# Performance work log

Hardware: AMD Instinct MI355X
Metric: run time of the kernel (lower is better)

The kernel has to match this reference:

```python
import jax, jax.numpy as jnp
import numpy as np

B, N, C, DIN, DOUT = 16, 65536, 256, 16, 16  # ratio = N // C = 256 nodes per cluster


def setup_inputs() -> dict:
    key = jax.random.key(0)
    k1, k2, k3, k4, k5 = jax.random.split(key, 5)
    stdv = 1.0 / np.sqrt(DOUT)
    x = jax.random.normal(k1, (B, N, DIN), dtype=jnp.float32)
    # parameters, pre-reshaped: torch w_diag (in*out, C) with out-major io axis -> (out, in, C)
    w_diag = jax.random.uniform(k2, (DOUT, DIN, C), jnp.float32, -stdv, stdv)
    w_off = jax.random.uniform(k3, (DOUT, DIN, C, C), jnp.float32, -stdv, stdv)
    b1 = jax.random.uniform(k4, (DOUT,), jnp.float32, -stdv, stdv)
    # flatten_ids(cluster_ids): a permutation putting each cluster's nodes contiguous
    permute_ids = jax.random.permutation(k5, N)
    return {"x": x, "w_diag": w_diag, "w_off": w_off, "b1": b1, "permute_ids": permute_ids}


def reference(x, w_diag, w_off, b1, permute_ids):
    # Faithful to: W = rearrange(kron(diag_embed(w_diag), I_r)) + (1/N) rearrange(kron(w_off, 1_{rxr}))
    # out = inv_permute( reshape( W @ flatten(permute(x)) ) ) + b1,
    # computed via the block-constant structure instead of materializing the (Dout*N, Din*N) W.
    Bq, Nn, Din = x.shape
    Dout, _, Cc = w_diag.shape
    ratio = Nn // Cc
    inv_permute = jnp.argsort(permute_ids)
    xp = x[:, permute_ids, :]                       # (B, N, Din), cluster-contiguous
    xc = xp.reshape(Bq, Cc, ratio, Din)             # (B, C, r, Din)
    # diagonal blocks: per-cluster Din->Dout mixing, identity over within-cluster index
    out_diag = jnp.einsum('oic,bcri->bcro', w_diag, xc)   # (B, C, r, Dout)
    # off blocks: constant within each (cluster j, cluster k) block -> use cluster sums
    s = xc.sum(axis=2)                              # (B, C, Din)
    out_off = jnp.einsum('oick,bki->bco', w_off, s) / Nn  # (B, C, Dout)
    out = out_diag + out_off[:, :, None, :]         # broadcast over within-cluster index
    out = out.reshape(Bq, Nn, Dout)[:, inv_permute, :] + b1[None, None, :]
    return out
```

## Files before the change

kernel.cpp:

```cpp
#include <hip/hip_runtime.h>

#define B_    16
#define N_    65536
#define C_    256
#define DIN_  16
#define DOUT_ 16
#define RATIO_ 256


__global__ __launch_bounds__(256) void k_cluster_sum(
    const float* __restrict__ x, const float* __restrict__ w_diag,
    const int* __restrict__ P, float* __restrict__ s, float* __restrict__ wd_t)
{
    int bid = blockIdx.x;
    int t = threadIdx.x;
    if (bid >= B_ * C_) {
        int c = bid - B_ * C_;
        int i = t >> 4, o = t & 15;
        wd_t[c * 256 + t] = w_diag[(o * DIN_ + i) * C_ + c];
        return;
    }
    int b = bid >> 8;
    int k = bid & (C_ - 1);
    int q  = t & 3;
    int rg = t >> 2;
    float4 acc = make_float4(0.f, 0.f, 0.f, 0.f);
    const int jbase = k * RATIO_;
    #pragma unroll
    for (int m = 0; m < 4; ++m) {
        int n = P[jbase + rg + 64 * m];
        const float4* row =
            reinterpret_cast<const float4*>(x + ((size_t)(b * N_ + n)) * DIN_);
        float4 v = row[q];
        acc.x += v.x; acc.y += v.y; acc.z += v.z; acc.w += v.w;
    }
    #pragma unroll
    for (int mask = 4; mask <= 32; mask <<= 1) {
        acc.x += __shfl_xor(acc.x, mask, 64);
        acc.y += __shfl_xor(acc.y, mask, 64);
        acc.z += __shfl_xor(acc.z, mask, 64);
        acc.w += __shfl_xor(acc.w, mask, 64);
    }
    __shared__ float4 part[4][4];
    int lane = t & 63, wave = t >> 6;
    if (lane < 4) part[wave][lane] = acc;
    __syncthreads();
    if (t < 16) {
        int qq = t >> 2, comp = t & 3;
        float v = 0.f;
        #pragma unroll
        for (int w = 0; w < 4; ++w) {
            const float* p = reinterpret_cast<const float*>(&part[w][qq]);
            v += p[comp];
        }
        int i = qq * 4 + comp;
        s[i * (B_ * C_) + b * C_ + k] = v;
    }
}

__global__ __launch_bounds__(256) void k_off(
    const float* __restrict__ w_off, const float* __restrict__ s,
    const float* __restrict__ b1, float* __restrict__ off)
{
    int c  = blockIdx.x >> 2;
    int og = blockIdx.x & 3;
    int t  = threadIdx.x;
    float acc[64];
    #pragma unroll
    for (int z = 0; z < 64; ++z) acc[z] = 0.f;

    for (int i = 0; i < DIN_; ++i) {
        float wv[4];
        #pragma unroll
        for (int o4 = 0; o4 < 4; ++o4) {
            int o = og * 4 + o4;
            wv[o4] = w_off[((size_t)((o * DIN_ + i) * C_ + c)) * C_ + t];
        }
        #pragma unroll
        for (int b = 0; b < B_; ++b) {
            float sv = s[i * (B_ * C_) + b * C_ + t];
            #pragma unroll
            for (int o4 = 0; o4 < 4; ++o4) acc[b * 4 + o4] += wv[o4] * sv;
        }
    }

    __shared__ float red[8][256];
    const float invN = 1.0f / (float)N_;
    #pragma unroll
    for (int rd = 0; rd < 8; ++rd) {
        __syncthreads();
        #pragma unroll
        for (int oo = 0; oo < 8; ++oo) red[oo][t] = acc[rd * 8 + oo];
        __syncthreads();
        int grp = t >> 5;
        int seg = t & 31;
        float p = 0.f;
        #pragma unroll
        for (int j = 0; j < 8; ++j) p += red[grp][seg * 8 + j];
        #pragma unroll
        for (int d = 16; d > 0; d >>= 1) p += __shfl_down(p, d, 32);
        if (seg == 0) {
            int outid = rd * 8 + grp;
            int b  = outid >> 2, o4 = outid & 3;
            int o  = og * 4 + o4;
            off[((b << 8) + c) * DOUT_ + o] = p * invN + b1[o];
        }
    }
}

__global__ __launch_bounds__(256) void k_apply(
    const float* __restrict__ x, const int* __restrict__ P,
    const float* __restrict__ wd_t, const float* __restrict__ off,
    float* __restrict__ out)
{
    int bid = blockIdx.x;
    int b = bid >> 8, k = bid & (C_ - 1);
    int t = threadIdx.x;
    __shared__ float4 wds[64];
    __shared__ float4 offs[4];
    reinterpret_cast<float*>(wds)[t] = wd_t[k * 256 + t];
    if (t < 16)
        reinterpret_cast<float*>(offs)[t] = off[((b << 8) + k) * DOUT_ + t];
    __syncthreads();

    int n = P[(k << 8) + t];
    const float4* row =
        reinterpret_cast<const float4*>(x + ((size_t)(b * N_ + n)) * DIN_);
    float4 x0 = row[0], x1 = row[1], x2 = row[2], x3 = row[3];
    float xv[16];
    xv[0]=x0.x; xv[1]=x0.y; xv[2]=x0.z; xv[3]=x0.w;
    xv[4]=x1.x; xv[5]=x1.y; xv[6]=x1.z; xv[7]=x1.w;
    xv[8]=x2.x; xv[9]=x2.y; xv[10]=x2.z; xv[11]=x2.w;
    xv[12]=x3.x; xv[13]=x3.y; xv[14]=x3.z; xv[15]=x3.w;

    float4 a0 = offs[0], a1 = offs[1], a2 = offs[2], a3 = offs[3];
    #pragma unroll
    for (int i = 0; i < 16; ++i) {
        float xi = xv[i];
        float4 w0 = wds[i * 4 + 0];
        float4 w1 = wds[i * 4 + 1];
        float4 w2 = wds[i * 4 + 2];
        float4 w3 = wds[i * 4 + 3];
        a0.x += xi * w0.x; a0.y += xi * w0.y; a0.z += xi * w0.z; a0.w += xi * w0.w;
        a1.x += xi * w1.x; a1.y += xi * w1.y; a1.z += xi * w1.z; a1.w += xi * w1.w;
        a2.x += xi * w2.x; a2.y += xi * w2.y; a2.z += xi * w2.z; a2.w += xi * w2.w;
        a3.x += xi * w3.x; a3.y += xi * w3.y; a3.z += xi * w3.z; a3.w += xi * w3.w;
    }
    float4* orow =
        reinterpret_cast<float4*>(out + ((size_t)(b * N_ + n)) * DOUT_);
    orow[0] = a0; orow[1] = a1; orow[2] = a2; orow[3] = a3;
}

extern "C" void kernel_launch(void* const* d_in, const int* in_sizes, int n_in,
                              void* d_out, int out_size, void* d_ws, size_t ws_size,
                              hipStream_t stream) {
    const float* x      = (const float*)d_in[0];
    const float* w_diag = (const float*)d_in[1];
    const float* w_off  = (const float*)d_in[2];
    const float* b1     = (const float*)d_in[3];
    const int*   P      = (const int*)d_in[4];
    float* out  = (float*)d_out;
    float* s    = (float*)d_ws;
    float* off  = s + 65536;
    float* wd_t = off + 65536;

    k_cluster_sum<<<B_ * C_ + C_, 256, 0, stream>>>(x, w_diag, P, s, wd_t);
    k_off<<<C_ * 4, 256, 0, stream>>>(w_off, s, b1, off);
    k_apply<<<B_ * C_, 256, 0, stream>>>(x, P, wd_t, off, out);
}
```

Before: 230.0 us.

## Fuse cluster sum into diagonal apply pass and add off-block term afterward

Merges the cluster-sum kernel with the diagonal Din->Dout apply so x is gathered only once, computing cluster sums from the same loaded rows via wave shuffles. The off-block contribution is then added in a separate streaming pass that uses a precomputed node-to-cluster map. This removes one gathered read of x but adds a full read-modify-write pass over the output plus a prep kernel building the inverse cluster map.

```diff
diff --git a/kernel.cpp b/kernel.cpp
--- a/kernel.cpp
+++ b/kernel.cpp
@@ -8,53 +8,98 @@
 #define RATIO_ 256
 
 
-__global__ __launch_bounds__(256) void k_cluster_sum(
-    const float* __restrict__ x, const float* __restrict__ w_diag,
-    const int* __restrict__ P, float* __restrict__ s, float* __restrict__ wd_t)
+__global__ __launch_bounds__(256) void k_prep(
+    const float* __restrict__ w_diag, const int* __restrict__ P,
+    float* __restrict__ wd_t, int* __restrict__ c_of_n)
+{
+    int t = threadIdx.x;
+    int bid = blockIdx.x;
+    if (bid < 256) {
+        int o = bid >> 4, i = bid & 15;
+        float v = w_diag[(o * DIN_ + i) * C_ + t];
+        wd_t[t * 256 + i * 16 + o] = v;
+    } else {
+        int k = bid - 256;
+        int j = k * 256 + t;
+        c_of_n[P[j]] = k;
+    }
+}
+
+__global__ __launch_bounds__(256) void k_main(
+    const float* __restrict__ x, const int* __restrict__ P,
+    const float* __restrict__ wd_t, float* __restrict__ s,
+    float* __restrict__ out)
 {
     int bid = blockIdx.x;
+    int b = bid >> 8, k = bid & (C_ - 1);
     int t = threadIdx.x;
-    if (bid >= B_ * C_) {
-        int c = bid - B_ * C_;
-        int i = t >> 4, o = t & 15;
-        wd_t[c * 256 + t] = w_diag[(o * DIN_ + i) * C_ + c];
-        return;
+    __shared__ float4 wds[64];
+    __shared__ float4 part[4][4];
+
+    reinterpret_cast<float*>(wds)[t] = wd_t[k * 256 + t];
+
+    int n = P[(k << 8) + t];
+    const float4* row =
+        reinterpret_cast<const float4*>(x + ((size_t)(b * N_ + n)) * DIN_);
+    float4 x0 = row[0], x1 = row[1], x2 = row[2], x3 = row[3];
+    __syncthreads();
+
+    float xv[16];
+    xv[0]=x0.x; xv[1]=x0.y; xv[2]=x0.z; xv[3]=x0.w;
+    xv[4]=x1.x; xv[5]=x1.y; xv[6]=x1.z; xv[7]=x1.w;
+    xv[8]=x2.x; xv[9]=x2.y; xv[10]=x2.z; xv[11]=x2.w;
+    xv[12]=x3.x; xv[13]=x3.y; xv[14]=x3.z; xv[15]=x3.w;
+
+    float4 a0 = make_float4(0.f,0.f,0.f,0.f), a1 = a0, a2 = a0, a3 = a0;
+    #pragma unroll
+    for (int i = 0; i < 16; ++i) {
+        float xi = xv[i];
+        float4 w0 = wds[i * 4 + 0];
+        float4 w1 = wds[i * 4 + 1];
+        float4 w2 = wds[i * 4 + 2];
+        float4 w3 = wds[i * 4 + 3];
+        a0.x += xi * w0.x; a0.y += xi * w0.y; a0.z += xi * w0.z; a0.w += xi * w0.w;
+        a1.x += xi * w1.x; a1.y += xi * w1.y; a1.z += xi * w1.z; a1.w += xi * w1.w;
+        a2.x += xi * w2.x; a2.y += xi * w2.y; a2.z += xi * w2.z; a2.w += xi * w2.w;
+        a3.x += xi * w3.x; a3.y += xi * w3.y; a3.z += xi * w3.z; a3.w += xi * w3.w;
     }
-    int b = bid >> 8;
-    int k = bid & (C_ - 1);
-    int q  = t & 3;
-    int rg = t >> 2;
-    float4 acc = make_float4(0.f, 0.f, 0.f, 0.f);
-    const int jbase = k * RATIO_;
+    float4* orow =
+        reinterpret_cast<float4*>(out + ((size_t)(b * N_ + n)) * DOUT_);
+    orow[0] = a0; orow[1] = a1; orow[2] = a2; orow[3] = a3;
+
     #pragma unroll
-    for (int m = 0; m < 4; ++m) {
-        int n = P[jbase + rg + 64 * m];
-        const float4* row =
-            reinterpret_cast<const float4*>(x + ((size_t)(b * N_ + n)) * DIN_);
-        float4 v = row[q];
-        acc.x += v.x; acc.y += v.y; acc.z += v.z; acc.w += v.w;
+    for (int mask = 1; mask <= 2; mask <<= 1) {
+        x0.x += __shfl_xor(x0.x, mask, 64); x0.y += __shfl_xor(x0.y, mask, 64);
+        x0.z += __shfl_xor(x0.z, mask, 64); x0.w += __shfl_xor(x0.w, mask, 64);
+        x1.x += __shfl_xor(x1.x, mask, 64); x1.y += __shfl_xor(x1.y, mask, 64);
+        x1.z += __shfl_xor(x1.z, mask, 64); x1.w += __shfl_xor(x1.w, mask, 64);
+        x2.x += __shfl_xor(x2.x, mask, 64); x2.y += __shfl_xor(x2.y, mask, 64);
+        x2.z += __shfl_xor(x2.z, mask, 64); x2.w += __shfl_xor(x2.w, mask, 64);
+        x3.x += __shfl_xor(x3.x, mask, 64); x3.y += __shfl_xor(x3.y, mask, 64);
+        x3.z += __shfl_xor(x3.z, mask, 64); x3.w += __shfl_xor(x3.w, mask, 64);
     }
+    int q = t & 3;
+    float4 v = (q == 0) ? x0 : (q == 1) ? x1 : (q == 2) ? x2 : x3;
     #pragma unroll
     for (int mask = 4; mask <= 32; mask <<= 1) {
-        acc.x += __shfl_xor(acc.x, mask, 64);
-        acc.y += __shfl_xor(acc.y, mask, 64);
-        acc.z += __shfl_xor(acc.z, mask, 64);
-        acc.w += __shfl_xor(acc.w, mask, 64);
+        v.x += __shfl_xor(v.x, mask, 64);
+        v.y += __shfl_xor(v.y, mask, 64);
+        v.z += __shfl_xor(v.z, mask, 64);
+        v.w += __shfl_xor(v.w, mask, 64);
     }
-    __shared__ float4 part[4][4];
     int lane = t & 63, wave = t >> 6;
-    if (lane < 4) part[wave][lane] = acc;
+    if (lane < 4) part[wave][lane] = v;
     __syncthreads();
     if (t < 16) {
         int qq = t >> 2, comp = t & 3;
-        float v = 0.f;
+        float sv = 0.f;
         #pragma unroll
         for (int w = 0; w < 4; ++w) {
             const float* p = reinterpret_cast<const float*>(&part[w][qq]);
-            v += p[comp];
+            sv += p[comp];
         }
         int i = qq * 4 + comp;
-        s[i * (B_ * C_) + b * C_ + k] = v;
+        s[i * (B_ * C_) + b * C_ + k] = sv;
     }
 }
 
@@ -108,47 +153,23 @@
     }
 }
 
-__global__ __launch_bounds__(256) void k_apply(
-    const float* __restrict__ x, const int* __restrict__ P,
-    const float* __restrict__ wd_t, const float* __restrict__ off,
+__global__ __launch_bounds__(256) void k_add_off(
+    const int* __restrict__ c_of_n, const float* __restrict__ off,
     float* __restrict__ out)
 {
-    int bid = blockIdx.x;
-    int b = bid >> 8, k = bid & (C_ - 1);
-    int t = threadIdx.x;
-    __shared__ float4 wds[64];
-    __shared__ float4 offs[4];
-    reinterpret_cast<float*>(wds)[t] = wd_t[k * 256 + t];
-    if (t < 16)
-        reinterpret_cast<float*>(offs)[t] = off[((b << 8) + k) * DOUT_ + t];
-    __syncthreads();
-
-    int n = P[(k << 8) + t];
-    const float4* row =
-        reinterpret_cast<const float4*>(x + ((size_t)(b * N_ + n)) * DIN_);
-    float4 x0 = row[0], x1 = row[1], x2 = row[2], x3 = row[3];
-    float xv[16];
-    xv[0]=x0.x; xv[1]=x0.y; xv[2]=x0.z; xv[3]=x0.w;
-    xv[4]=x1.x; xv[5]=x1.y; xv[6]=x1.z; xv[7]=x1.w;
-    xv[8]=x2.x; xv[9]=x2.y; xv[10]=x2.z; xv[11]=x2.w;
-    xv[12]=x3.x; xv[13]=x3.y; xv[14]=x3.z; xv[15]=x3.w;
-
-    float4 a0 = offs[0], a1 = offs[1], a2 = offs[2], a3 = offs[3];
-    #pragma unroll
-    for (int i = 0; i < 16; ++i) {
-        float xi = xv[i];
-        float4 w0 = wds[i * 4 + 0];
-        float4 w1 = wds[i * 4 + 1];
-        float4 w2 = wds[i * 4 + 2];
-        float4 w3 = wds[i * 4 + 3];
-        a0.x += xi * w0.x; a0.y += xi * w0.y; a0.z += xi * w0.z; a0.w += xi * w0.w;
-        a1.x += xi * w1.x; a1.y += xi * w1.y; a1.z += xi * w1.z; a1.w += xi * w1.w;
-        a2.x += xi * w2.x; a2.y += xi * w2.y; a2.z += xi * w2.z; a2.w += xi * w2.w;
-        a3.x += xi * w3.x; a3.y += xi * w3.y; a3.z += xi * w3.z; a3.w += xi * w3.w;
-    }
-    float4* orow =
-        reinterpret_cast<float4*>(out + ((size_t)(b * N_ + n)) * DOUT_);
-    orow[0] = a0; orow[1] = a1; orow[2] = a2; orow[3] = a3;
+    size_t g = (size_t)blockIdx.x * 256 + threadIdx.x;
+    int rowid = (int)(g >> 2);
+    int b = rowid >> 16;
+    int n = rowid & 65535;
+    int q = (int)(g & 3);
+    int c = c_of_n[n];
+    const float4* offp =
+        reinterpret_cast<const float4*>(off + (size_t)(((b << 8) + c) * DOUT_));
+    float4 o4 = offp[q];
+    float4* op = reinterpret_cast<float4*>(out) + g;
+    float4 v = *op;
+    v.x += o4.x; v.y += o4.y; v.z += o4.z; v.w += o4.w;
+    *op = v;
 }
 
 extern "C" void kernel_launch(void* const* d_in, const int* in_sizes, int n_in,
@@ -159,12 +180,14 @@
     const float* w_off  = (const float*)d_in[2];
     const float* b1     = (const float*)d_in[3];
     const int*   P      = (const int*)d_in[4];
-    float* out  = (float*)d_out;
-    float* s    = (float*)d_ws;
-    float* off  = s + 65536;
-    float* wd_t = off + 65536;
+    float* out    = (float*)d_out;
+    float* s      = (float*)d_ws;
+    float* off    = s + 65536;
+    float* wd_t   = off + 65536;
+    int*   c_of_n = (int*)(wd_t + 65536);
 
-    k_cluster_sum<<<B_ * C_ + C_, 256, 0, stream>>>(x, w_diag, P, s, wd_t);
+    k_prep<<<512, 256, 0, stream>>>(w_diag, P, wd_t, c_of_n);
+    k_main<<<B_ * C_, 256, 0, stream>>>(x, P, wd_t, s, out);
     k_off<<<C_ * 4, 256, 0, stream>>>(w_off, s, b1, off);
-    k_apply<<<B_ * C_, 256, 0, stream>>>(x, P, wd_t, off, out);
+    k_add_off<<<(B_ * N_ * DOUT_ / 4) / 256, 256, 0, stream>>>(c_of_n, off, out);
 }
```

Result: no change. 226.6 us (-1.5%).
